# Optimization experiments

Measured on AMD Instinct MI355X. Metric: run time of the kernel, lower is better.

## Reference

```python
import jax, jax.numpy as jnp
import numpy as np

B, T, C = 2, 2048, 1024
H = 16
HS = C // H  # 64
LN_EPS = 1e-5

def setup_inputs() -> dict:
    key = jax.random.key(0)
    ks = jax.random.split(key, 12)
    s = lambda *sh: 0.02
    inp = {
        'x': jax.random.normal(ks[0], (B, T, C), jnp.float32),
        # per-head Q/K/V weights (bias=False), stacked over heads: [H, C, HS]
        'wq': jax.random.normal(ks[1], (H, C, HS), jnp.float32) * 0.02,
        'wk': jax.random.normal(ks[2], (H, C, HS), jnp.float32) * 0.02,
        'wv': jax.random.normal(ks[3], (H, C, HS), jnp.float32) * 0.02,
        'w_proj': jax.random.normal(ks[4], (C, C), jnp.float32) * 0.02,
        'b_proj': jnp.zeros((C,), jnp.float32),
        'w1': jax.random.normal(ks[5], (C, 4 * C), jnp.float32) * 0.02,
        'b1': jnp.zeros((4 * C,), jnp.float32),
        'w2': jax.random.normal(ks[6], (4 * C, C), jnp.float32) * 0.02,
        'b2': jnp.zeros((C,), jnp.float32),
        'ln1_g': jnp.ones((C,), jnp.float32),
        'ln1_b': jnp.zeros((C,), jnp.float32),
        'ln2_g': jnp.ones((C,), jnp.float32),
        'ln2_b': jnp.zeros((C,), jnp.float32),
    }
    return inp

def _layernorm(x, g, b):
    mu = jnp.mean(x, axis=-1, keepdims=True)
    var = jnp.mean(jnp.square(x - mu), axis=-1, keepdims=True)
    return (x - mu) * jax.lax.rsqrt(var + LN_EPS) * g + b

def reference(x, wq, wk, wv, w_proj, b_proj, w1, b1, w2, b2, ln1_g, ln1_b, ln2_g, ln2_b):
    Bx, Tx, Cx = x.shape
    h = _layernorm(x, ln1_g, ln1_b)
    q = jnp.einsum('btc,hcd->bhtd', h, wq)
    k = jnp.einsum('btc,hcd->bhtd', h, wk)
    v = jnp.einsum('btc,hcd->bhtd', h, wv)
    # NOTE: original scales by n_embedding**-0.5 (C), not head_size**-0.5
    scores = jnp.einsum('bhtd,bhsd->bhts', q, k) * (Cx ** -0.5)
    causal = jnp.tril(jnp.ones((Tx, Tx), bool))
    scores = jnp.where(causal, scores, -jnp.inf)
    att = jax.nn.softmax(scores, axis=-1)  # [B,H,T,T]
    out = jnp.einsum('bhts,bhsd->bhtd', att, v)
    out = out.transpose(0, 2, 1, 3).reshape(Bx, Tx, Cx)  # concat heads
    out = out @ w_proj + b_proj
    x = x + out
    h2 = _layernorm(x, ln2_g, ln2_b)
    ff = jax.nn.relu(h2 @ w1 + b1) @ w2 + b2
    return x + ff
```

## Files before the change

### kernel.cpp

```cpp
#include <hip/hip_runtime.h>
#include <hip/hip_bf16.h>
#include <stdint.h>

typedef __bf16 bf16_t;
typedef __bf16 bf16x8 __attribute__((ext_vector_type(8)));
typedef __bf16 bf16x4 __attribute__((ext_vector_type(4)));
typedef float f32x4 __attribute__((ext_vector_type(4)));

static constexpr int TT = 2048, CC = 1024;

__device__ __forceinline__ void gld_lds16(const void* g, void* l) {
  __builtin_amdgcn_global_load_lds((const __attribute__((address_space(1))) void*)g,
                                   (__attribute__((address_space(3))) void*)l, 16, 0, 0);
}

__global__ __launch_bounds__(256) void transpose_cvt(const float* __restrict__ in,
                                                     bf16_t* __restrict__ out,
                                                     int K, int N) {
  __shared__ float t[32][33];
  const int k0 = blockIdx.x * 32, n0 = blockIdx.y * 32;
  const size_t boff = (size_t)blockIdx.z * K * N;
  in += boff;
  out += boff;
  const int tx = threadIdx.x & 31, ty = threadIdx.x >> 5;
#pragma unroll
  for (int j = 0; j < 4; ++j)
    t[ty + j * 8][tx] = in[(size_t)(k0 + ty + j * 8) * N + n0 + tx];
  __syncthreads();
#pragma unroll
  for (int j = 0; j < 4; ++j)
    out[(size_t)(n0 + ty + j * 8) * K + k0 + tx] = (bf16_t)t[tx][ty + j * 8];
}

__global__ __launch_bounds__(256) void ln_f32_bf16(const float* __restrict__ x,
                                                   const float* __restrict__ g,
                                                   const float* __restrict__ b,
                                                   bf16_t* __restrict__ out) {
  const int row = blockIdx.x;
  const int tid = threadIdx.x;
  const float4 v = ((const float4*)(x + (size_t)row * CC))[tid];
  float s = v.x + v.y + v.z + v.w;
  float q = v.x * v.x + v.y * v.y + v.z * v.z + v.w * v.w;
#pragma unroll
  for (int off = 1; off < 64; off <<= 1) {
    s += __shfl_xor(s, off);
    q += __shfl_xor(q, off);
  }
  __shared__ float red[8];
  const int wave = tid >> 6, lane = tid & 63;
  if (lane == 0) { red[wave] = s; red[4 + wave] = q; }
  __syncthreads();
  s = red[0] + red[1] + red[2] + red[3];
  q = red[4] + red[5] + red[6] + red[7];
  const float mu = s * (1.0f / CC);
  float var = q * (1.0f / CC) - mu * mu;
  var = fmaxf(var, 0.f);
  const float rstd = rsqrtf(var + 1e-5f);
  const float4 gv = ((const float4*)g)[tid];
  const float4 bv = ((const float4*)b)[tid];
  bf16x4 o;
  o[0] = (bf16_t)((v.x - mu) * rstd * gv.x + bv.x);
  o[1] = (bf16_t)((v.y - mu) * rstd * gv.y + bv.y);
  o[2] = (bf16_t)((v.z - mu) * rstd * gv.z + bv.z);
  o[3] = (bf16_t)((v.w - mu) * rstd * gv.w + bv.w);
  *(bf16x4*)(out + (size_t)row * CC + tid * 4) = o;
}

template <int EPI, int BN>
__global__ __launch_bounds__(256) void gemm_bt(const bf16_t* __restrict__ A,
                                               const bf16_t* __restrict__ Bt,
                                               void* __restrict__ Cout,
                                               const float* __restrict__ bias,
                                               const float* __restrict__ res,
                                               bf16_t* __restrict__ vt,
                                               int M, int N, int K) {
  constexpr int WN = BN / 2;
  constexpr int NF = BN / 32;
  constexpr int NB = BN / 32;
  __shared__ alignas(16) bf16_t As[2][128 * 64];
  __shared__ alignas(16) bf16_t Bs[2][BN * 64];
  const int tid = threadIdx.x;
  const int wave = tid >> 6, lane = tid & 63;
  const int lr = lane & 15, lg = lane >> 4;
  const int wm = wave >> 1, wn = wave & 1;
  const int tm0 = blockIdx.y * 128, tn0 = blockIdx.x * BN;

  const int sr = lane >> 3;
  const int scs = (lane & 7) ^ sr;
  const bf16_t* Ag[4];
#pragma unroll
  for (int i = 0; i < 4; ++i)
    Ag[i] = A + (size_t)(tm0 + i * 32 + wave * 8 + sr) * K + scs * 8;
  const bf16_t* Bg[NB];
#pragma unroll
  for (int i = 0; i < NB; ++i)
    Bg[i] = Bt + (size_t)(tn0 + i * 32 + wave * 8 + sr) * K + scs * 8;

  auto STAGE = [&](int k0, bf16_t* Ad, bf16_t* Bd) {
#pragma unroll
    for (int i = 0; i < 4; ++i)
      gld_lds16(Ag[i] + k0, Ad + (i * 32 + wave * 8) * 64);
#pragma unroll
    for (int i = 0; i < NB; ++i)
      gld_lds16(Bg[i] + k0, Bd + (i * 32 + wave * 8) * 64);
  };

  f32x4 acc[4][NF] = {};
  const int NT = K >> 6;

  STAGE(0, As[0], Bs[0]);
  asm volatile("s_waitcnt vmcnt(0)" ::: "memory");
  __builtin_amdgcn_s_barrier();

  for (int t = 0; t < NT; ++t) {
    const int cur = t & 1;
    bf16_t* Ac = As[cur];
    bf16_t* Bc = Bs[cur];
    if (t + 1 < NT) STAGE((t + 1) << 6, As[cur ^ 1], Bs[cur ^ 1]);

    bf16x8 af[2][4], bfr[2][NF];
#pragma unroll
    for (int kk = 0; kk < 2; ++kk) {
      const int ch = ((kk * 4 + lg) ^ (lr & 7)) * 8;
#pragma unroll
      for (int m = 0; m < 4; ++m)
        af[kk][m] = *(const bf16x8*)&Ac[(wm * 64 + m * 16 + lr) * 64 + ch];
#pragma unroll
      for (int n = 0; n < NF; ++n)
        bfr[kk][n] = *(const bf16x8*)&Bc[(wn * WN + n * 16 + lr) * 64 + ch];
    }
    asm volatile("s_waitcnt lgkmcnt(0)" ::: "memory");
    __builtin_amdgcn_sched_barrier(0);
    __builtin_amdgcn_s_setprio(1);
#pragma unroll
    for (int kk = 0; kk < 2; ++kk)
#pragma unroll
      for (int m = 0; m < 4; ++m)
#pragma unroll
        for (int n = 0; n < NF; ++n)
          acc[m][n] =
              __builtin_amdgcn_mfma_f32_16x16x32_bf16(af[kk][m], bfr[kk][n], acc[m][n], 0, 0, 0);
    __builtin_amdgcn_s_setprio(0);
    asm volatile("s_waitcnt vmcnt(0)" ::: "memory");
    __builtin_amdgcn_sched_barrier(0);
    __builtin_amdgcn_s_barrier();
  }

#pragma unroll
  for (int m = 0; m < 4; ++m) {
#pragma unroll
    for (int i = 0; i < 4; ++i) {
      const int row = tm0 + wm * 64 + m * 16 + lg * 4 + i;
#pragma unroll
      for (int n = 0; n < NF; ++n) {
        const int col = tn0 + wn * WN + n * 16 + lr;
        float v = acc[m][n][i];
        if (EPI == 1) v = fmaxf(v + bias[col], 0.f);
        if (EPI == 2) v = v + bias[col] + res[(size_t)row * N + col];
        if (EPI == 2) {
          ((float*)Cout)[(size_t)row * N + col] = v;
        } else if (EPI == 3) {
          if (col >= 2048) {
            const int hd = col - 2048;
            const size_t vidx =
                ((size_t)((row >> 11) * 16 + (hd >> 6)) * 64 + (hd & 63)) * TT + (row & (TT - 1));
            vt[vidx] = (bf16_t)v;
          } else {
            ((bf16_t*)Cout)[(size_t)row * N + col] = (bf16_t)v;
          }
        } else {
          ((bf16_t*)Cout)[(size_t)row * N + col] = (bf16_t)v;
        }
      }
    }
  }
}

__global__ __launch_bounds__(256, 3) void attn_fwd(const bf16_t* __restrict__ qkv,
                                                   const bf16_t* __restrict__ Vt,
                                                   bf16_t* __restrict__ O) {
  const int bh = blockIdx.x;
  const int bb = bh >> 4, hh = bh & 15;
  const int qt = 31 - (int)blockIdx.y;
  const int qbase = qt * 64;
  const int tid = threadIdx.x;
  const int wave = tid >> 6, lane = tid & 63;
  const int lr = lane & 15, lg = lane >> 4;
  const bf16_t* Qp = qkv + (size_t)bb * TT * 3072 + hh * 64;
  const bf16_t* Kp = Qp + 1024;
  const bf16_t* Vh = Vt + (size_t)bh * 64 * TT;

  constexpr int KLP = 72;
  constexpr int VLP = 136;
  constexpr int PLP = 136;
  __shared__ alignas(16) bf16_t Klds[128 * KLP];
  __shared__ alignas(16) bf16_t Vlds[64 * VLP];
  __shared__ alignas(16) bf16_t PlS[4][16 * PLP];
  bf16_t* Pw = PlS[wave];

  const int ksr = wave * 32 + (lane >> 3);
  const int ksc = (lane & 7) * 8;
  const int vsr = wave * 16 + (lane >> 4);
  const int vsc = (lane & 15) * 8;

  const int qrow = qbase + wave * 16;
  bf16x8 qf0, qf1;
  {
    const bf16x8 a = *(const bf16x8*)(Qp + (size_t)(qrow + lr) * 3072 + lg * 8);
    const bf16x8 b = *(const bf16x8*)(Qp + (size_t)(qrow + lr) * 3072 + 32 + lg * 8);
#pragma unroll
    for (int j = 0; j < 8; ++j) {
      qf0[j] = (bf16_t)((float)a[j] * 0.03125f);
      qf1[j] = (bf16_t)((float)b[j] * 0.03125f);
    }
  }

  f32x4 oacc[4] = {};
  float m_r[4], l_r[4];
#pragma unroll
  for (int i = 0; i < 4; ++i) { m_r[i] = -1e38f; l_r[i] = 0.f; }

  bf16x8 kpre[4], vpre[4];
#pragma unroll
  for (int i = 0; i < 4; ++i) {
    kpre[i] = *(const bf16x8*)(Kp + (size_t)(ksr + i * 8) * 3072 + ksc);
    vpre[i] = *(const bf16x8*)(Vh + (size_t)(vsr + i * 4) * TT + vsc);
  }
#pragma unroll
  for (int i = 0; i < 4; ++i) {
    *(bf16x8*)&Klds[(ksr + i * 8) * KLP + ksc] = kpre[i];
    *(bf16x8*)&Vlds[(vsr + i * 4) * VLP + vsc] = vpre[i];
  }
  __syncthreads();

  const int nt = (qt >> 1) + 1;
  for (int t = 0; t < nt; ++t) {
    const int s0 = t * 128;
    const int sn = (t + 1 < nt) ? s0 + 128 : s0;
#pragma unroll
    for (int i = 0; i < 4; ++i) {
      kpre[i] = *(const bf16x8*)(Kp + (size_t)(sn + ksr + i * 8) * 3072 + ksc);
      vpre[i] = *(const bf16x8*)(Vh + (size_t)(vsr + i * 4) * TT + sn + vsc);
    }

    const int u = (qrow - s0) >> 4;
    const int cmc = min(u | 1, 7);

    float P[8][4];
    __builtin_amdgcn_s_setprio(1);
#pragma unroll
    for (int ct = 0; ct < 8; ++ct) {
      if (ct <= cmc) {
        const bf16x8 kf0 = *(const bf16x8*)&Klds[(ct * 16 + lr) * KLP + lg * 8];
        const bf16x8 kf1 = *(const bf16x8*)&Klds[(ct * 16 + lr) * KLP + 32 + lg * 8];
        f32x4 z = {};
        z = __builtin_amdgcn_mfma_f32_16x16x32_bf16(qf0, kf0, z, 0, 0, 0);
        z = __builtin_amdgcn_mfma_f32_16x16x32_bf16(qf1, kf1, z, 0, 0, 0);
        if (ct >= u) {
          const int sg = s0 + ct * 16 + lr;
#pragma unroll
          for (int i = 0; i < 4; ++i)
            P[ct][i] = (sg > qrow + lg * 4 + i) ? -1e30f : z[i];
        } else {
#pragma unroll
          for (int i = 0; i < 4; ++i) P[ct][i] = z[i];
        }
      } else {
#pragma unroll
        for (int i = 0; i < 4; ++i) P[ct][i] = -1e30f;
      }
    }
    __builtin_amdgcn_s_setprio(0);

    float lmax[4];
#pragma unroll
    for (int i = 0; i < 4; ++i) {
      float m0 = fmaxf(fmaxf(P[0][i], P[1][i]), fmaxf(P[2][i], P[3][i]));
      float m1 = fmaxf(fmaxf(P[4][i], P[5][i]), fmaxf(P[6][i], P[7][i]));
      lmax[i] = fmaxf(m0, m1);
    }
    const bool ok = (lmax[0] <= m_r[0] + 8.f) && (lmax[1] <= m_r[1] + 8.f) &&
                    (lmax[2] <= m_r[2] + 8.f) && (lmax[3] <= m_r[3] + 8.f);
    if (!__all(ok)) {
      float rm[4] = {lmax[0], lmax[1], lmax[2], lmax[3]};
#pragma unroll
      for (int off = 1; off < 16; off <<= 1)
#pragma unroll
        for (int i = 0; i < 4; ++i) rm[i] = fmaxf(rm[i], __shfl_xor(rm[i], off));
#pragma unroll
      for (int i = 0; i < 4; ++i) {
        const float mn = fmaxf(m_r[i], rm[i]);
        const float alpha = __expf(m_r[i] - mn);
        m_r[i] = mn;
        l_r[i] *= alpha;
#pragma unroll
        for (int db = 0; db < 4; ++db) oacc[db][i] *= alpha;
      }
    }

#pragma unroll
    for (int i = 0; i < 4; ++i) {
      float ls = 0.f;
#pragma unroll
      for (int ct = 0; ct < 8; ++ct) {
        const float p = __expf(P[ct][i] - m_r[i]);
        P[ct][i] = p;
        ls += p;
      }
      l_r[i] += ls;
    }

#pragma unroll
    for (int ct = 0; ct < 8; ++ct) {
      if (ct <= cmc) {
#pragma unroll
        for (int i = 0; i < 4; ++i) {
          const int q = lg * 4 + i;
          const int col = (ct * 16 + lr) ^ ((lg >> 1) << 4);
          Pw[q * PLP + col] = (bf16_t)P[ct][i];
        }
      }
    }
    asm volatile("s_waitcnt lgkmcnt(0)" ::: "memory");
    __builtin_amdgcn_sched_barrier(0);

    const int kcm = cmc >> 1;
    __builtin_amdgcn_s_setprio(1);
#pragma unroll
    for (int kc = 0; kc < 4; ++kc) {
      if (kc <= kcm) {
        const bf16x8 pf =
            *(const bf16x8*)&Pw[lr * PLP + ((kc * 32 + lg * 8) ^ ((lr >> 3) << 4))];
#pragma unroll
        for (int db = 0; db < 4; ++db) {
          const bf16x8 vf = *(const bf16x8*)&Vlds[(db * 16 + lr) * VLP + kc * 32 + lg * 8];
          oacc[db] = __builtin_amdgcn_mfma_f32_16x16x32_bf16(pf, vf, oacc[db], 0, 0, 0);
        }
      }
    }
    __builtin_amdgcn_s_setprio(0);

    if (t + 1 < nt) {
      __syncthreads();
#pragma unroll
      for (int i = 0; i < 4; ++i) {
        *(bf16x8*)&Klds[(ksr + i * 8) * KLP + ksc] = kpre[i];
        *(bf16x8*)&Vlds[(vsr + i * 4) * VLP + vsc] = vpre[i];
      }
      __syncthreads();
    }
  }

#pragma unroll
  for (int off = 1; off < 16; off <<= 1)
#pragma unroll
    for (int i = 0; i < 4; ++i) l_r[i] += __shfl_xor(l_r[i], off);

  bf16_t* Op = O + ((size_t)bb * TT + qrow) * CC + hh * 64;
#pragma unroll
  for (int i = 0; i < 4; ++i) {
    const float rl = 1.0f / l_r[i];
#pragma unroll
    for (int db = 0; db < 4; ++db)
      Op[(size_t)(lg * 4 + i) * CC + db * 16 + lr] = (bf16_t)(oacc[db][i] * rl);
  }
}

extern "C" void kernel_launch(void* const* d_in, const int* in_sizes, int n_in,
                              void* d_out, int out_size, void* d_ws, size_t ws_size,
                              hipStream_t stream) {
  const float* x      = (const float*)d_in[0];
  const float* wq     = (const float*)d_in[1];
  const float* wk     = (const float*)d_in[2];
  const float* wv     = (const float*)d_in[3];
  const float* w_proj = (const float*)d_in[4];
  const float* b_proj = (const float*)d_in[5];
  const float* w1     = (const float*)d_in[6];
  const float* b1     = (const float*)d_in[7];
  const float* w2     = (const float*)d_in[8];
  const float* b2     = (const float*)d_in[9];
  const float* ln1_g  = (const float*)d_in[10];
  const float* ln1_b  = (const float*)d_in[11];
  const float* ln2_g  = (const float*)d_in[12];
  const float* ln2_b  = (const float*)d_in[13];

  char* ws = (char*)d_ws;
  const size_t MB = 1024 * 1024;
  bf16_t* h1    = (bf16_t*)(ws + 0);
  bf16_t* Bqkv  = (bf16_t*)(ws + 8 * MB);
  bf16_t* Bproj = (bf16_t*)(ws + 14 * MB);
  bf16_t* B1w   = (bf16_t*)(ws + 16 * MB);
  bf16_t* B2w   = (bf16_t*)(ws + 24 * MB);
  bf16_t* qkv   = (bf16_t*)(ws + 32 * MB);
  bf16_t* Obuf  = (bf16_t*)(ws + 56 * MB);
  float*  res1  = (float*)(ws + 64 * MB);
  bf16_t* Vt    = (bf16_t*)(ws + 64 * MB);
  bf16_t* h2    = (bf16_t*)(ws + 80 * MB);
  bf16_t* a1    = (bf16_t*)(ws + 32 * MB);
  float*  outp  = (float*)d_out;

  dim3 blk(256);
  transpose_cvt<<<dim3(32, 2, 16), blk, 0, stream>>>(wq, Bqkv, 1024, 64);
  transpose_cvt<<<dim3(32, 2, 16), blk, 0, stream>>>(wk, Bqkv + 1024 * 1024, 1024, 64);
  transpose_cvt<<<dim3(32, 2, 16), blk, 0, stream>>>(wv, Bqkv + 2 * 1024 * 1024, 1024, 64);
  transpose_cvt<<<dim3(32, 32, 1), blk, 0, stream>>>(w_proj, Bproj, 1024, 1024);
  transpose_cvt<<<dim3(32, 128, 1), blk, 0, stream>>>(w1, B1w, 1024, 4096);
  transpose_cvt<<<dim3(128, 32, 1), blk, 0, stream>>>(w2, B2w, 4096, 1024);

  ln_f32_bf16<<<dim3(4096), blk, 0, stream>>>(x, ln1_g, ln1_b, h1);
  gemm_bt<3, 128><<<dim3(24, 32), blk, 0, stream>>>(h1, Bqkv, qkv, nullptr, nullptr, Vt,
                                                    4096, 3072, 1024);
  attn_fwd<<<dim3(32, 32), blk, 0, stream>>>(qkv, Vt, Obuf);
  gemm_bt<2, 64><<<dim3(16, 32), blk, 0, stream>>>(Obuf, Bproj, res1, b_proj, x, nullptr,
                                                   4096, 1024, 1024);
  ln_f32_bf16<<<dim3(4096), blk, 0, stream>>>(res1, ln2_g, ln2_b, h2);
  gemm_bt<1, 128><<<dim3(32, 32), blk, 0, stream>>>(h2, B1w, a1, b1, nullptr, nullptr,
                                                    4096, 4096, 1024);
  gemm_bt<2, 64><<<dim3(16, 32), blk, 0, stream>>>(a1, B2w, outp, b2, res1, nullptr,
                                                   4096, 1024, 4096);
}
```

Baseline: 256.6 us.

## Add triple-buffered LDS pipeline for narrow GEMMs and XCD-aware block remapping

Templates the GEMM on pipeline depth and uses three LDS stages for the BN=64 projection and FFN-down GEMMs, waiting only on the oldest stage's loads via a partial vmcnt. It also remaps workgroup IDs so consecutive tiles land on the same XCD (stride-8 swizzle), aiming to improve L2 reuse of A/B tiles. The extra buffer raises LDS use, which may lower occupancy, and the remap assumes the workgroup count divides by 8.

After: 258.7 us. About the same (+0.8%).

```diff
diff --git a/kernel.cpp b/kernel.cpp
--- a/kernel.cpp
+++ b/kernel.cpp
@@ -66,7 +66,7 @@
   *(bf16x4*)(out + (size_t)row * CC + tid * 4) = o;
 }
 
-template <int EPI, int BN>
+template <int EPI, int BN, int DEPTH>
 __global__ __launch_bounds__(256) void gemm_bt(const bf16_t* __restrict__ A,
                                                const bf16_t* __restrict__ Bt,
                                                void* __restrict__ Cout,
@@ -77,13 +77,18 @@
   constexpr int WN = BN / 2;
   constexpr int NF = BN / 32;
   constexpr int NB = BN / 32;
-  __shared__ alignas(16) bf16_t As[2][128 * 64];
-  __shared__ alignas(16) bf16_t Bs[2][BN * 64];
+  __shared__ alignas(16) bf16_t As[DEPTH][128 * 64];
+  __shared__ alignas(16) bf16_t Bs[DEPTH][BN * 64];
   const int tid = threadIdx.x;
   const int wave = tid >> 6, lane = tid & 63;
   const int lr = lane & 15, lg = lane >> 4;
   const int wm = wave >> 1, wn = wave & 1;
-  const int tm0 = blockIdx.y * 128, tn0 = blockIdx.x * BN;
+
+  const int gx = gridDim.x;
+  const int nwg = gx * gridDim.y;
+  const int orig = (int)blockIdx.y * gx + (int)blockIdx.x;
+  const int wgid = (orig & 7) * (nwg >> 3) + (orig >> 3);
+  const int tm0 = (wgid / gx) * 128, tn0 = (wgid % gx) * BN;
 
   const int sr = lane >> 3;
   const int scs = (lane & 7) ^ sr;
@@ -96,27 +101,33 @@
   for (int i = 0; i < NB; ++i)
     Bg[i] = Bt + (size_t)(tn0 + i * 32 + wave * 8 + sr) * K + scs * 8;
 
-  auto STAGE = [&](int k0, bf16_t* Ad, bf16_t* Bd) {
+  auto STAGE = [&](int k0, int buf) {
 #pragma unroll
     for (int i = 0; i < 4; ++i)
-      gld_lds16(Ag[i] + k0, Ad + (i * 32 + wave * 8) * 64);
+      gld_lds16(Ag[i] + k0, &As[buf][(i * 32 + wave * 8) * 64]);
 #pragma unroll
     for (int i = 0; i < NB; ++i)
-      gld_lds16(Bg[i] + k0, Bd + (i * 32 + wave * 8) * 64);
+      gld_lds16(Bg[i] + k0, &Bs[buf][(i * 32 + wave * 8) * 64]);
   };
 
   f32x4 acc[4][NF] = {};
   const int NT = K >> 6;
 
-  STAGE(0, As[0], Bs[0]);
-  asm volatile("s_waitcnt vmcnt(0)" ::: "memory");
+  STAGE(0, 0);
+  if (DEPTH == 3 && NT > 1) {
+    STAGE(64, 1);
+    asm volatile("s_waitcnt vmcnt(%0)" ::"i"(4 + NB) : "memory");
+  } else {
+    asm volatile("s_waitcnt vmcnt(0)" ::: "memory");
+  }
   __builtin_amdgcn_s_barrier();
 
   for (int t = 0; t < NT; ++t) {
-    const int cur = t & 1;
-    bf16_t* Ac = As[cur];
-    bf16_t* Bc = Bs[cur];
-    if (t + 1 < NT) STAGE((t + 1) << 6, As[cur ^ 1], Bs[cur ^ 1]);
+    const int cur = t % DEPTH;
+    const bf16_t* Ac = As[cur];
+    const bf16_t* Bc = Bs[cur];
+    const bool more = (t + DEPTH - 1) < NT;
+    if (more) STAGE((t + DEPTH - 1) << 6, (t + DEPTH - 1) % DEPTH);
 
     bf16x8 af[2][4], bfr[2][NF];
 #pragma unroll
@@ -141,7 +152,11 @@
           acc[m][n] =
               __builtin_amdgcn_mfma_f32_16x16x32_bf16(af[kk][m], bfr[kk][n], acc[m][n], 0, 0, 0);
     __builtin_amdgcn_s_setprio(0);
-    asm volatile("s_waitcnt vmcnt(0)" ::: "memory");
+    if (DEPTH == 3 && more) {
+      asm volatile("s_waitcnt vmcnt(%0)" ::"i"(4 + NB) : "memory");
+    } else {
+      asm volatile("s_waitcnt vmcnt(0)" ::: "memory");
+    }
     __builtin_amdgcn_sched_barrier(0);
     __builtin_amdgcn_s_barrier();
   }
@@ -408,14 +423,14 @@
   transpose_cvt<<<dim3(128, 32, 1), blk, 0, stream>>>(w2, B2w, 4096, 1024);
 
   ln_f32_bf16<<<dim3(4096), blk, 0, stream>>>(x, ln1_g, ln1_b, h1);
-  gemm_bt<3, 128><<<dim3(24, 32), blk, 0, stream>>>(h1, Bqkv, qkv, nullptr, nullptr, Vt,
-                                                    4096, 3072, 1024);
+  gemm_bt<3, 128, 2><<<dim3(24, 32), blk, 0, stream>>>(h1, Bqkv, qkv, nullptr, nullptr, Vt,
+                                                       4096, 3072, 1024);
   attn_fwd<<<dim3(32, 32), blk, 0, stream>>>(qkv, Vt, Obuf);
-  gemm_bt<2, 64><<<dim3(16, 32), blk, 0, stream>>>(Obuf, Bproj, res1, b_proj, x, nullptr,
-                                                   4096, 1024, 1024);
+  gemm_bt<2, 64, 3><<<dim3(16, 32), blk, 0, stream>>>(Obuf, Bproj, res1, b_proj, x, nullptr,
+                                                      4096, 1024, 1024);
   ln_f32_bf16<<<dim3(4096), blk, 0, stream>>>(res1, ln2_g, ln2_b, h2);
-  gemm_bt<1, 128><<<dim3(32, 32), blk, 0, stream>>>(h2, B1w, a1, b1, nullptr, nullptr,
-                                                    4096, 4096, 1024);
-  gemm_bt<2, 64><<<dim3(16, 32), blk, 0, stream>>>(a1, B2w, outp, b2, res1, nullptr,
-                                                   4096, 1024, 4096);
-}
+  gemm_bt<1, 128, 2><<<dim3(32, 32), blk, 0, stream>>>(h2, B1w, a1, b1, nullptr, nullptr,
+                                                       4096, 4096, 1024);
+  gemm_bt<2, 64, 3><<<dim3(16, 32), blk, 0, stream>>>(a1, B2w, outp, b2, res1, nullptr,
+                                                      4096, 1024, 4096);
+}
```
